# Performance work log

Hardware: AMD Instinct MI355X
Metric: run time of the kernel (lower is better)

The kernel has to match this reference:

```python
import jax, jax.numpy as jnp
import numpy as np

MIN_SCORE = 0.3       # min_score_threshold
NMS_THRESHOLD = 0.3   # nms_threshold
MAX_OUT = 256         # fixed output padding (jit-compatible replacement for dynamic K)


def _cxcywh_to_xyxy(b):
    cx, cy, w, h = b[..., 0], b[..., 1], b[..., 2], b[..., 3]
    half_w, half_h = w * 0.5, h * 0.5
    return jnp.stack([cx - half_w, cy - half_h, cx + half_w, cy + half_h], axis=-1)


def _pairwise_iou(a, b):
    # a: [N,4], b: [M,4] in xyxy
    lt = jnp.maximum(a[:, None, :2], b[None, :, :2])
    rb = jnp.minimum(a[:, None, 2:], b[None, :, 2:])
    wh = jnp.clip(rb - lt, 0.0)
    inter = wh[..., 0] * wh[..., 1]
    area_a = (a[:, 2] - a[:, 0]) * (a[:, 3] - a[:, 1])
    area_b = (b[:, 2] - b[:, 0]) * (b[:, 3] - b[:, 1])
    return inter / (area_a[:, None] + area_b[None, :] - inter + 1e-9)


def setup_inputs() -> dict:
    key = jax.random.key(0)
    k1, k2 = jax.random.split(key)
    N, n_coords = 8192, 16
    score = jax.random.uniform(k1, (N, 1), dtype=jnp.float32)
    box = jax.random.uniform(k2, (N, n_coords), dtype=jnp.float32)
    return {"score": score, "box": box}


def reference(score, box):
    # score: [N,1], box: [N,n_coords]; single class (n_classes==1, cls=None)
    s = score[:, 0]
    valid = s >= MIN_SCORE                      # score mask applied before NMS
    order = jnp.argsort(-s)                     # score-descending (batched_nms order)
    s_s = s[order]
    v_s = valid[order]
    box_s = box[order]
    bbox = _cxcywh_to_xyxy(box_s[:, :4]).astype(jnp.float32)
    iou = _pairwise_iou(bbox, bbox)             # [N,N]
    N = s.shape[0]

    def body(kept, i):
        # suppressed if overlaps any already-kept (higher-score) box
        suppressed = jnp.any(kept & (iou[:, i] > NMS_THRESHOLD))
        keep_i = v_s[i] & jnp.logical_not(suppressed)
        return kept.at[i].set(keep_i), None

    kept, _ = jax.lax.scan(body, jnp.zeros((N,), dtype=bool), jnp.arange(N))

    # compact kept detections to the front, preserving score order (stable sort)
    comp = jnp.argsort(jnp.where(kept, 0, 1), stable=True)[:MAX_OUT]
    out_valid = kept[comp]                      # [MAX_OUT]
    score_out = jnp.where(out_valid[:, None], s_s[comp][:, None], 0.0)   # [MAX_OUT,1]
    box_out = jnp.where(out_valid[:, None], box_s[comp], 0.0)            # [MAX_OUT,n_coords]
    return score_out, box_out, out_valid
```

## Files before the change

### kernel.cpp

```cpp
#include <hip/hip_runtime.h>
#include <stdint.h>

typedef unsigned long long u64;

#define N 8192
#define NW 128
#define MAX_OUT 256
#define MASK_BYTES ((size_t)N * NW * 8)


__global__ __launch_bounds__(1024)
void rank_fused_kernel(const float* __restrict__ score, const float* __restrict__ box,
                       int* __restrict__ order, float* __restrict__ s_s,
                       float4* __restrict__ bbox, float* __restrict__ area,
                       int* __restrict__ nvalid) {
    __shared__ uint32_t ksc[N];
    __shared__ int psum[32][33];
    __shared__ int vpart[16];
    const int tid = threadIdx.x;

    const float4* s4 = (const float4*)score;
    float4 a = s4[tid * 2], b = s4[tid * 2 + 1];
    ksc[tid * 8 + 0] = __float_as_uint(a.x);
    ksc[tid * 8 + 1] = __float_as_uint(a.y);
    ksc[tid * 8 + 2] = __float_as_uint(a.z);
    ksc[tid * 8 + 3] = __float_as_uint(a.w);
    ksc[tid * 8 + 4] = __float_as_uint(b.x);
    ksc[tid * 8 + 5] = __float_as_uint(b.y);
    ksc[tid * 8 + 6] = __float_as_uint(b.z);
    ksc[tid * 8 + 7] = __float_as_uint(b.w);
    int c = (a.x >= 0.3f) + (a.y >= 0.3f) + (a.z >= 0.3f) + (a.w >= 0.3f)
          + (b.x >= 0.3f) + (b.y >= 0.3f) + (b.z >= 0.3f) + (b.w >= 0.3f);
    for (int off = 32; off; off >>= 1) c += __shfl_down(c, off);
    if ((tid & 63) == 0) vpart[tid >> 6] = c;
    __syncthreads();
    if (blockIdx.x == 0 && tid == 0) {
        int t = 0;
        #pragma unroll
        for (int w = 0; w < 16; ++w) t += vpart[w];
        *nvalid = t;
    }

    const int i_local = tid & 31;
    const int jg = tid >> 5;
    const int ibase = blockIdx.x * 32;
    const uint32_t si = ksc[ibase + i_local];
    const int i = ibase + i_local;
    int cnt = 0;
    const int j0 = jg * 256;
    #pragma unroll 8
    for (int t = 0; t < 256; ++t) {
        const int j = j0 + t;
        const uint32_t sj = ksc[j];
        cnt += (sj > si || (sj == si && j < i)) ? 1 : 0;
    }
    psum[i_local][jg] = cnt;
    __syncthreads();

    if (tid < 32) {
        int r = 0;
        #pragma unroll
        for (int k = 0; k < 32; ++k) r += psum[tid][k];
        const int ii = ibase + tid;
        order[r] = ii;
        s_s[r] = score[ii];
        float4 cb = ((const float4*)box)[ii * 4];
        float hw = cb.z * 0.5f, hh = cb.w * 0.5f;
        float x0 = cb.x - hw, y0 = cb.y - hh, x1 = cb.x + hw, y1 = cb.y + hh;
        bbox[r] = make_float4(x0, y0, x1, y1);
        area[r] = (x1 - x0) * (y1 - y0);
    }
}

__global__ __launch_bounds__(256)
void mask_kernel(const float4* __restrict__ bbox, const float* __restrict__ area,
                 const int* __restrict__ nvalid_p, u64* __restrict__ maskT) {
    const int w = blockIdx.x;
    if (w < (int)(blockIdx.y << 2)) return;
    const int nv = *nvalid_p;
    if ((int)(blockIdx.y * 256) >= nv) return;
    __shared__ float4 jb[64];
    __shared__ float  ja[64];
    if (threadIdx.x < 64) {
        jb[threadIdx.x] = bbox[w * 64 + threadIdx.x];
        ja[threadIdx.x] = area[w * 64 + threadIdx.x];
    }
    __syncthreads();
    const int i = blockIdx.y * 256 + threadIdx.x;
    if (i >= nv) return;
    if (w < (i >> 6)) return;
    float4 aa4 = bbox[i];
    float  aa = area[i];
    u64 bits = 0, fb = 0;
    #pragma unroll 8
    for (int jj = 0; jj < 64; ++jj) {
        float4 b = jb[jj];
        float lx = fmaxf(aa4.x, b.x), ly = fmaxf(aa4.y, b.y);
        float rx = fminf(aa4.z, b.z), ry = fminf(aa4.w, b.w);
        float ww = fmaxf(rx - lx, 0.0f), hh = fmaxf(ry - ly, 0.0f);
        float inter = ww * hh;
        float denom = ((aa + ja[jj]) - inter) + 1e-9f;
        float d = fmaf(-0.3f, denom, inter);
        bits |= ((u64)(d > 0.0f)) << jj;
        fb   |= ((u64)(fabsf(d) <= 1e-5f * denom)) << jj;
    }
    if (fb) {
        while (fb) {
            int jj = (int)__builtin_ctzll(fb); fb &= fb - 1;
            float4 b = jb[jj];
            float lx = fmaxf(aa4.x, b.x), ly = fmaxf(aa4.y, b.y);
            float rx = fminf(aa4.z, b.z), ry = fminf(aa4.w, b.w);
            float ww = fmaxf(rx - lx, 0.0f), hh = fmaxf(ry - ly, 0.0f);
            float inter = ww * hh;
            float denom = ((aa + ja[jj]) - inter) + 1e-9f;
            float iou = inter / denom;
            bits = (bits & ~(1ull << jj)) | (((u64)(iou > 0.3f)) << jj);
        }
    }
    maskT[(size_t)w * N + i] = bits;
}

struct Pipe { u64 col, s1, s2, g0, g1, g2, g3; };

__device__ __forceinline__ unsigned or_dpp32(unsigned v) {
    v |= (unsigned)__builtin_amdgcn_update_dpp(0, (int)v, 0x111, 0xf, 0xf, true);
    v |= (unsigned)__builtin_amdgcn_update_dpp(0, (int)v, 0x112, 0xf, 0xf, true);
    v |= (unsigned)__builtin_amdgcn_update_dpp(0, (int)v, 0x114, 0xf, 0xf, true);
    v |= (unsigned)__builtin_amdgcn_update_dpp(0, (int)v, 0x118, 0xf, 0xf, true);
    v |= (unsigned)__builtin_amdgcn_update_dpp(0, (int)v, 0x142, 0xf, 0xf, true);
    v |= (unsigned)__builtin_amdgcn_update_dpp(0, (int)v, 0x143, 0xf, 0xf, true);
    return v;
}

__device__ __forceinline__ u64 wave_or64(u64 v) {
    unsigned lo = or_dpp32((unsigned)v);
    unsigned hi = or_dpp32((unsigned)(v >> 32));
    unsigned slo = (unsigned)__builtin_amdgcn_readlane((int)lo, 63);
    unsigned shi = (unsigned)__builtin_amdgcn_readlane((int)hi, 63);
    return ((u64)shi << 32) | (u64)slo;
}

__global__ __launch_bounds__(64)
void nms_kernel(const u64* __restrict__ maskT, const float* __restrict__ s_s,
                const int* __restrict__ order, const float* __restrict__ box,
                const int* __restrict__ nvalid_p, float* __restrict__ out) {
    const int lane = threadIdx.x;
    const int nv = *nvalid_p;
    const int nblk = (nv + 63) >> 6;
    __shared__ int kpos[MAX_OUT];
    int kcount = 0;
    u64 s1m = 0, s2m = 0, s2m_old = 0;

    Pipe A, B;
    A.col = A.s1 = A.s2 = A.g0 = A.g1 = A.g2 = A.g3 = 0;
    B.col = B.s1 = B.s2 = B.g0 = B.g1 = B.g2 = B.g3 = 0;
    if (nblk > 0) {
        A.col = maskT[lane];
        if (nblk > 1) A.s1 = maskT[(size_t)1 * N + lane];
        if (nblk > 2) A.s2 = maskT[(size_t)2 * N + lane];
    }
    if (nblk > 1) {
        B.col = maskT[(size_t)1 * N + 64 + lane];
        if (nblk > 2) B.s1 = maskT[(size_t)2 * N + 64 + lane];
        if (nblk > 3) B.s2 = maskT[(size_t)3 * N + 64 + lane];
    }

    auto step = [&](int b, Pipe& P) -> bool {
        u64 col = P.col, s1v = P.s1, s2v = P.s2;
        u64 x = P.g0 | P.g1 | P.g2 | P.g3 | s1m | s2m_old;
        const int b2 = b + 2;
        P.col = P.s1 = P.s2 = P.g0 = P.g1 = P.g2 = P.g3 = 0;
        if (b2 < nblk) {
            const int row = (b2 << 6) + lane;
            P.col = maskT[(size_t)b2 * N + row];
            if (b2 + 1 < nblk) P.s1 = maskT[(size_t)(b2 + 1) * N + row];
            if (b2 + 2 < nblk) P.s2 = maskT[(size_t)(b2 + 2) * N + row];
            const int kc = kcount;
            const u64* colw = maskT + (size_t)b2 * N;
            if (lane < kc)       P.g0 = colw[kpos[lane]];
            if (lane +  64 < kc) P.g1 = colw[kpos[lane +  64]];
            if (lane + 128 < kc) P.g2 = colw[kpos[lane + 128]];
            if (lane + 192 < kc) P.g3 = colw[kpos[lane + 192]];
        }
        u64 rw = wave_or64(x);
        const int base = b << 6;
        const int rem = nv - base;
        u64 validm = (rem >= 64) ? ~0ull : ((1ull << rem) - 1ull);
        u64 todo = validm & ~rw;
        u64 km = 0;
        while (todo) {
            int l = (int)__builtin_ctzll(todo);
            u64 row_l = __ballot(((col >> l) & 1ull) != 0);
            if (lane == 0) kpos[kcount] = base + l;
            km |= (1ull << l);
            kcount++;
            todo &= ~row_l;
            todo &= ~(1ull << l);
            if (kcount >= MAX_OUT) break;
        }
        u64 keepm = ((km >> lane) & 1ull) ? ~0ull : 0ull;
        s2m_old = s2m;
        s2m = s2v & keepm;
        s1m = s1v & keepm;
        return kcount < MAX_OUT;
    };

    bool run = true;
    for (int b = 0; run && b < nblk; b += 2) {
        run = step(b, A);
        if (run && b + 1 < nblk) run = step(b + 1, B);
    }

    __syncthreads();
    float* out_score = out;
    float* out_box   = out + MAX_OUT;
    float* out_valid = out + MAX_OUT + MAX_OUT * 16;
    const float4* box4 = (const float4*)box;
    float4* ob4 = (float4*)out_box;
    for (int t = lane; t < MAX_OUT; t += 64) {
        if (t < kcount) {
            int p = kpos[t];
            out_score[t] = s_s[p];
            out_valid[t] = 1.0f;
            int oi = order[p];
            #pragma unroll
            for (int q = 0; q < 4; ++q) ob4[t * 4 + q] = box4[oi * 4 + q];
        } else {
            out_score[t] = 0.0f;
            out_valid[t] = 0.0f;
            float4 z = make_float4(0.f, 0.f, 0.f, 0.f);
            #pragma unroll
            for (int q = 0; q < 4; ++q) ob4[t * 4 + q] = z;
        }
    }
}

extern "C" void kernel_launch(void* const* d_in, const int* in_sizes, int n_in,
                              void* d_out, int out_size, void* d_ws, size_t ws_size,
                              hipStream_t stream) {
    const float* score = (const float*)d_in[0];
    const float* box   = (const float*)d_in[1];
    char* ws = (char*)d_ws;
    u64*    maskT  = (u64*)ws;
    int*    order  = (int*)   (ws + MASK_BYTES);
    float*  s_s    = (float*) (ws + MASK_BYTES + 32768);
    float4* bbox   = (float4*)(ws + MASK_BYTES + 65536);
    float*  area   = (float*) (ws + MASK_BYTES + 65536 + 131072);
    int*    nvalid = (int*)   (ws + MASK_BYTES + 65536 + 131072 + 32768);

    rank_fused_kernel<<<256, 1024, 0, stream>>>(score, box, order, s_s, bbox, area, nvalid);
    mask_kernel<<<dim3(128, 32), 256, 0, stream>>>(bbox, area, nvalid, maskT);
    nms_kernel<<<1, 64, 0, stream>>>(maskT, s_s, order, box, nvalid, (float*)d_out);
}
```

Baseline: 124.2 us.

## Accumulate kept-row suppression masks per lane instead of gathering per block

Replaces the per-block gather of kept-box columns plus the wave-wide OR reduction with a running per-lane removal vector. Each lane owns two 64-bit mask words and ORs in the rows of newly kept boxes, and the block's suppression word is fetched with a single readlane. Near-diagonal suppression for the next two blocks is handled by scalar readlanes of the prefetched s1/s2 words, and row loads are deferred through three rotating register sets. The intent is to shorten the serial dependency chain per block. In exchange it raises register pressure, adds scalar readlane loops proportional to the number of kept boxes, and makes the macro-heavy code harder to follow.

```diff
diff --git a/kernel.cpp b/kernel.cpp
--- a/kernel.cpp
+++ b/kernel.cpp
@@ -120,25 +120,59 @@
     maskT[(size_t)w * N + i] = bits;
 }
 
-struct Pipe { u64 col, s1, s2, g0, g1, g2, g3; };
-
-__device__ __forceinline__ unsigned or_dpp32(unsigned v) {
-    v |= (unsigned)__builtin_amdgcn_update_dpp(0, (int)v, 0x111, 0xf, 0xf, true);
-    v |= (unsigned)__builtin_amdgcn_update_dpp(0, (int)v, 0x112, 0xf, 0xf, true);
-    v |= (unsigned)__builtin_amdgcn_update_dpp(0, (int)v, 0x114, 0xf, 0xf, true);
-    v |= (unsigned)__builtin_amdgcn_update_dpp(0, (int)v, 0x118, 0xf, 0xf, true);
-    v |= (unsigned)__builtin_amdgcn_update_dpp(0, (int)v, 0x142, 0xf, 0xf, true);
-    v |= (unsigned)__builtin_amdgcn_update_dpp(0, (int)v, 0x143, 0xf, 0xf, true);
-    return v;
-}
-
-__device__ __forceinline__ u64 wave_or64(u64 v) {
-    unsigned lo = or_dpp32((unsigned)v);
-    unsigned hi = or_dpp32((unsigned)(v >> 32));
-    unsigned slo = (unsigned)__builtin_amdgcn_readlane((int)lo, 63);
-    unsigned shi = (unsigned)__builtin_amdgcn_readlane((int)hi, 63);
-    return ((u64)shi << 32) | (u64)slo;
-}
+
+#define RL64(v, l) ( ((u64)(unsigned)__builtin_amdgcn_readlane((int)(unsigned)((v) >> 32), (l)) << 32) \
+                   |  (u64)(unsigned)__builtin_amdgcn_readlane((int)(unsigned)(v), (l)) )
+
+#define NMS_STEP(B, PC, PS1, PS2, R0,R1,R2,R3,R4,R5,R6,R7) do {               \
+    const int b_ = (B);                                                        \
+                \
+    remv0 |= R0 | R2 | R4 | R6;                                                \
+    remv1 |= R1 | R3 | R5 | R7;                                                \
+    u64 rwv_ = (b_ < 64) ? remv0 : remv1;                                      \
+    u64 rw_ = RL64(rwv_, b_ & 63) | rsup;                                      \
+    u64 col_ = PC, s1v_ = PS1, s2v_ = PS2;                                     \
+    PC = 0; PS1 = 0; PS2 = 0;                                                  \
+    const int b2_ = b_ + 2;                                                    \
+    if (b2_ < nblk) {                                                          \
+        const int row_ = (b2_ << 6) + lane;                                    \
+        PC = maskT[(size_t)b2_ * N + row_];                                    \
+        if (b2_ + 1 < nblk) PS1 = maskT[(size_t)(b2_ + 1) * N + row_];         \
+        if (b2_ + 2 < nblk) PS2 = maskT[(size_t)(b2_ + 2) * N + row_];         \
+    }                                                                          \
+    const int base_ = b_ << 6;                                                 \
+    const int rem_ = nv - base_;                                               \
+    u64 validm_ = (rem_ >= 64) ? ~0ull : ((1ull << rem_) - 1ull);              \
+    u64 todo_ = validm_ & ~rw_;                                                \
+    u64 km_ = 0;                                                               \
+    while (todo_) {                                                            \
+        int l_ = (int)__builtin_ctzll(todo_);                                  \
+        u64 rowl_ = __ballot(((col_ >> l_) & 1ull) != 0);                      \
+        if (lane == 0) kpos[kcount] = base_ + l_;                              \
+        km_ |= (1ull << l_); kcount++;                                         \
+        todo_ &= ~rowl_; todo_ &= ~(1ull << l_);                               \
+        if (kcount >= MAX_OUT) break;                                          \
+    }                                                                          \
+             \
+    u64 a1_ = 0, a2_ = 0, t_ = km_;                                            \
+    while (t_) { int l_ = (int)__builtin_ctzll(t_); t_ &= t_ - 1;              \
+                 a1_ |= RL64(s1v_, l_); a2_ |= RL64(s2v_, l_); }               \
+    rsup = carry | a1_; carry = a2_;                                           \
+         \
+    R0=0;R1=0;R2=0;R3=0;R4=0;R5=0;R6=0;R7=0;                                   \
+    u64 t2_ = km_;                                                             \
+    if (t2_) { int r_ = base_ + (int)__builtin_ctzll(t2_); t2_ &= t2_ - 1;     \
+               R0 = maskT[woff0 + r_]; R1 = maskT[woff1 + r_]; }               \
+    if (t2_) { int r_ = base_ + (int)__builtin_ctzll(t2_); t2_ &= t2_ - 1;     \
+               R2 = maskT[woff0 + r_]; R3 = maskT[woff1 + r_]; }               \
+    if (t2_) { int r_ = base_ + (int)__builtin_ctzll(t2_); t2_ &= t2_ - 1;     \
+               R4 = maskT[woff0 + r_]; R5 = maskT[woff1 + r_]; }               \
+    if (t2_) { int r_ = base_ + (int)__builtin_ctzll(t2_); t2_ &= t2_ - 1;     \
+               R6 = maskT[woff0 + r_]; R7 = maskT[woff1 + r_]; }               \
+    while (t2_) { int r_ = base_ + (int)__builtin_ctzll(t2_); t2_ &= t2_ - 1;  \
+                  remv0 |= maskT[woff0 + r_]; remv1 |= maskT[woff1 + r_]; }    \
+    run = (kcount < MAX_OUT);                                                  \
+} while (0)
 
 __global__ __launch_bounds__(64)
 void nms_kernel(const u64* __restrict__ maskT, const float* __restrict__ s_s,
@@ -149,66 +183,39 @@
     const int nblk = (nv + 63) >> 6;
     __shared__ int kpos[MAX_OUT];
     int kcount = 0;
-    u64 s1m = 0, s2m = 0, s2m_old = 0;
-
-    Pipe A, B;
-    A.col = A.s1 = A.s2 = A.g0 = A.g1 = A.g2 = A.g3 = 0;
-    B.col = B.s1 = B.s2 = B.g0 = B.g1 = B.g2 = B.g3 = 0;
+
+    u64 remv0 = 0, remv1 = 0, rsup = 0, carry = 0;
+    u64 ra0=0,ra1=0,ra2=0,ra3=0,ra4=0,ra5=0,ra6=0,ra7=0;
+    u64 rb0=0,rb1=0,rb2=0,rb3=0,rb4=0,rb5=0,rb6=0,rb7=0;
+    u64 rc0=0,rc1=0,rc2=0,rc3=0,rc4=0,rc5=0,rc6=0,rc7=0;
+    u64 pac=0,pas1=0,pas2=0,pbc=0,pbs1=0,pbs2=0;
+    const size_t woff0 = (size_t)lane * N;
+    const size_t woff1 = (size_t)(64 + lane) * N;
+
     if (nblk > 0) {
-        A.col = maskT[lane];
-        if (nblk > 1) A.s1 = maskT[(size_t)1 * N + lane];
-        if (nblk > 2) A.s2 = maskT[(size_t)2 * N + lane];
+        pac = maskT[lane];
+        if (nblk > 1) pas1 = maskT[(size_t)1 * N + lane];
+        if (nblk > 2) pas2 = maskT[(size_t)2 * N + lane];
     }
     if (nblk > 1) {
-        B.col = maskT[(size_t)1 * N + 64 + lane];
-        if (nblk > 2) B.s1 = maskT[(size_t)2 * N + 64 + lane];
-        if (nblk > 3) B.s2 = maskT[(size_t)3 * N + 64 + lane];
-    }
-
-    auto step = [&](int b, Pipe& P) -> bool {
-        u64 col = P.col, s1v = P.s1, s2v = P.s2;
-        u64 x = P.g0 | P.g1 | P.g2 | P.g3 | s1m | s2m_old;
-        const int b2 = b + 2;
-        P.col = P.s1 = P.s2 = P.g0 = P.g1 = P.g2 = P.g3 = 0;
-        if (b2 < nblk) {
-            const int row = (b2 << 6) + lane;
-            P.col = maskT[(size_t)b2 * N + row];
-            if (b2 + 1 < nblk) P.s1 = maskT[(size_t)(b2 + 1) * N + row];
-            if (b2 + 2 < nblk) P.s2 = maskT[(size_t)(b2 + 2) * N + row];
-            const int kc = kcount;
-            const u64* colw = maskT + (size_t)b2 * N;
-            if (lane < kc)       P.g0 = colw[kpos[lane]];
-            if (lane +  64 < kc) P.g1 = colw[kpos[lane +  64]];
-            if (lane + 128 < kc) P.g2 = colw[kpos[lane + 128]];
-            if (lane + 192 < kc) P.g3 = colw[kpos[lane + 192]];
-        }
-        u64 rw = wave_or64(x);
-        const int base = b << 6;
-        const int rem = nv - base;
-        u64 validm = (rem >= 64) ? ~0ull : ((1ull << rem) - 1ull);
-        u64 todo = validm & ~rw;
-        u64 km = 0;
-        while (todo) {
-            int l = (int)__builtin_ctzll(todo);
-            u64 row_l = __ballot(((col >> l) & 1ull) != 0);
-            if (lane == 0) kpos[kcount] = base + l;
-            km |= (1ull << l);
-            kcount++;
-            todo &= ~row_l;
-            todo &= ~(1ull << l);
-            if (kcount >= MAX_OUT) break;
-        }
-        u64 keepm = ((km >> lane) & 1ull) ? ~0ull : 0ull;
-        s2m_old = s2m;
-        s2m = s2v & keepm;
-        s1m = s1v & keepm;
-        return kcount < MAX_OUT;
-    };
+        pbc = maskT[(size_t)1 * N + 64 + lane];
+        if (nblk > 2) pbs1 = maskT[(size_t)2 * N + 64 + lane];
+        if (nblk > 3) pbs2 = maskT[(size_t)3 * N + 64 + lane];
+    }
 
     bool run = true;
-    for (int b = 0; run && b < nblk; b += 2) {
-        run = step(b, A);
-        if (run && b + 1 < nblk) run = step(b + 1, B);
+    for (int b6 = 0; run && b6 < nblk; b6 += 6) {
+        NMS_STEP(b6 + 0, pac, pas1, pas2, ra0,ra1,ra2,ra3,ra4,ra5,ra6,ra7);
+        if (run && b6 + 1 < nblk)
+            NMS_STEP(b6 + 1, pbc, pbs1, pbs2, rb0,rb1,rb2,rb3,rb4,rb5,rb6,rb7);
+        if (run && b6 + 2 < nblk)
+            NMS_STEP(b6 + 2, pac, pas1, pas2, rc0,rc1,rc2,rc3,rc4,rc5,rc6,rc7);
+        if (run && b6 + 3 < nblk)
+            NMS_STEP(b6 + 3, pbc, pbs1, pbs2, ra0,ra1,ra2,ra3,ra4,ra5,ra6,ra7);
+        if (run && b6 + 4 < nblk)
+            NMS_STEP(b6 + 4, pac, pas1, pas2, rb0,rb1,rb2,rb3,rb4,rb5,rb6,rb7);
+        if (run && b6 + 5 < nblk)
+            NMS_STEP(b6 + 5, pbc, pbs1, pbs2, rc0,rc1,rc2,rc3,rc4,rc5,rc6,rc7);
     }
 
     __syncthreads();
```

Result: slower. 172.9 us (+39.2%).
